# Kernel tuning notes

Measured on AMD Instinct MI355X. Metric: run time of the kernel, lower is better.

The kernel has to match this reference:

```python
import jax, jax.numpy as jnp
import numpy as np

C = 2048
RED = 8
D = C // RED  # 256


def setup_inputs() -> dict:
    key = jax.random.key(0)
    ks = jax.random.split(key, 8)
    n, h, w = 4, 64, 64
    x = jax.random.normal(ks[0], (n, C, h, w), dtype=jnp.float32)
    # 1x1 conv weights stored as [out_ch, in_ch]
    w1 = jax.random.normal(ks[1], (D, C), dtype=jnp.float32) * 0.02
    b1 = jnp.zeros((D,), dtype=jnp.float32)
    w2 = jax.random.normal(ks[2], (D, C), dtype=jnp.float32) * 0.02
    b2 = jnp.zeros((D,), dtype=jnp.float32)
    w3 = jax.random.normal(ks[3], (C, C), dtype=jnp.float32) * 0.02
    b3 = jnp.zeros((C,), dtype=jnp.float32)
    alpha = jnp.zeros((1,), dtype=jnp.float32)
    return {"x": x, "w1": w1, "b1": b1, "w2": w2, "b2": b2,
            "w3": w3, "b3": b3, "alpha": alpha}


def reference(x, w1, b1, w2, b2, w3, b3, alpha):
    n, c, h, w = x.shape
    hw = h * w
    xf = x.reshape(n, c, hw)  # [n, C, HW]
    # 1x1 convs == per-position matmuls over channels
    e1 = jax.nn.relu(jnp.einsum('dc,ncp->ndp', w1, xf) + b1[None, :, None])  # [n, D, HW]
    e2 = jax.nn.relu(jnp.einsum('dc,ncp->ndp', w2, xf) + b2[None, :, None])  # [n, D, HW]
    assembly = jax.nn.relu(jnp.einsum('oc,ncp->nop', w3, xf) + b3[None, :, None])  # [n, C, HW]
    # attention[i, j] = softmax_j( e1[:, i] . e2[:, j] )
    scores = jnp.einsum('ndi,ndj->nij', e1, e2)  # [n, HW, HW]
    attn = jax.nn.softmax(scores, axis=-1)
    # torch.bmm(x, attn^T): out[:, :, i] = sum_j x[:, :, j] * attn[i, j]
    out = jnp.einsum('ncj,nij->nci', xf, attn)  # [n, C, HW]
    y = alpha[0] * out + assembly
    return y.reshape(n, c, h, w)
```

## Files before the change

kernel.cpp:

```cpp
#include <hip/hip_runtime.h>
#include <math.h>

#define CC 2048
#define DD 256
#define PP 4096
#define NB 4

typedef float f32x4 __attribute__((ext_vector_type(4)));
typedef __bf16 bfrag __attribute__((ext_vector_type(8)));

#define AS1(p) ((const __attribute__((address_space(1))) void*)(p))
#define AS3(p) ((__attribute__((address_space(3))) void*)(p))

__device__ __forceinline__ unsigned short f2bf(float f) {
    unsigned int u = __float_as_uint(f);
    u = (u + 0x7fffu + ((u >> 16) & 1u)) >> 16;
    return (unsigned short)u;
}

__global__ __launch_bounds__(256) void prep(const float* __restrict__ x, unsigned short* __restrict__ xT,
                                            const float* __restrict__ w3, unsigned short* __restrict__ w3b) {
    const int t = threadIdx.x;
    if (blockIdx.z == NB) {
        int bid = blockIdx.y * 64 + blockIdx.x;
        int base = (bid * 256 + t) * 8;
#pragma unroll
        for (int j = 0; j < 2; ++j) {
            float4 v = *(const float4*)(w3 + base + j * 4);
            ushort4 r;
            r.x = f2bf(v.x); r.y = f2bf(v.y); r.z = f2bf(v.z); r.w = f2bf(v.w);
            *(ushort4*)(w3b + base + j * 4) = r;
        }
        return;
    }
    __shared__ float tile[64 * 64];
    const int n  = blockIdx.z;
    const int c0 = blockIdx.y * 64;
    const int p0 = blockIdx.x * 64;
    const float* xn = x + (size_t)n * CC * PP;
    {
        const int cl = t >> 4;
        const int g  = t & 15;
        const int pl = g * 4;
#pragma unroll
        for (int ps = 0; ps < 4; ++ps) {
            const int c = cl + ps * 16;
            float4 v = *(const float4*)(xn + (size_t)(c0 + c) * PP + p0 + pl);
            const int gs = g ^ (c >> 2);
            *(float4*)(tile + c * 64 + gs * 4) = v;
        }
    }
    __syncthreads();
    unsigned short* xTn = xT + (size_t)n * PP * CC;
    {
        const int pl2 = t >> 4;
        const int cq  = t & 15;
        const int c4  = cq * 4;
#pragma unroll
        for (int ps = 0; ps < 4; ++ps) {
            const int p  = pl2 + ps * 16;
            const int gs2 = (p >> 2) ^ cq;
            const int base = gs2 * 4 + (p & 3);
            ushort4 r;
            r.x = f2bf(tile[(c4 + 0) * 64 + base]);
            r.y = f2bf(tile[(c4 + 1) * 64 + base]);
            r.z = f2bf(tile[(c4 + 2) * 64 + base]);
            r.w = f2bf(tile[(c4 + 3) * 64 + base]);
            *(ushort4*)(xTn + (size_t)(p0 + p) * CC + c0 + c4) = r;
        }
    }
}

__global__ __launch_bounds__(512, 2) void gemm_assembly(
    const unsigned short* __restrict__ w3b,
    const unsigned short* __restrict__ xT,
    const float* __restrict__ b3,
    float* __restrict__ out)
{
    __shared__ __align__(16) char sm[131072];

    const int t    = threadIdx.x;
    const int wave = t >> 6;
    const int lane = t & 63;
    const int swz  = lane & 7;

    const int p0 = blockIdx.x << 8;
    const int m0 = blockIdx.y << 8;
    const int nb = blockIdx.z;

    const int rA = t >> 3;
    const int g  = (t & 7) ^ (rA & 7);
    const unsigned short* Ag = w3b + (size_t)(m0 + rA) * CC + g * 8;
    const unsigned short* Bg = xT + (size_t)nb * PP * CC + (size_t)(p0 + rA) * CC + g * 8;
    const int ldsw = wave << 10;

    const char* Abase = sm + ((wave >> 2) << 14) + (lane & 15) * 128;
    const char* Bbase = sm + 65536 + (((wave & 3) >> 1) << 14) + ((wave & 1) << 13) + (lane & 15) * 128;

    const int ck0 = (((lane >> 4) ^ swz) << 4);
    const int ck1 = ck0 ^ 0x40;

    f32x4 acc[8][4];
#pragma unroll
    for (int i = 0; i < 8; ++i)
#pragma unroll
        for (int j = 0; j < 4; ++j)
            acc[i][j] = (f32x4){0.f, 0.f, 0.f, 0.f};

    bfrag a0k0, a0k1, a1k0, a1k1, a2k0, a2k1, a3k0, a3k1;
    bfrag bA0k0, bA0k1, bA1k0, bA1k1;
    bfrag bB0k0, bB0k1, bB1k0, bB1k1;

#define STG(SB, DO, kt, h) do { \
    const unsigned short* _s = (SB) + (size_t)(h) * 128 * CC + (size_t)(kt) * 64; \
    char* _d = sm + (DO) + (((kt) & 1) << 15) + ((h) << 14) + ldsw; \
    __builtin_amdgcn_global_load_lds(AS1(_s), AS3(_d), 16, 0, 0); \
    __builtin_amdgcn_global_load_lds(AS1(_s + 64 * CC), AS3(_d + 8192), 16, 0, 0); \
} while (0)

#define LD(dst, BASE, OFF) dst = *(const bfrag*)((BASE) + (OFF))
#define Q(I, J, A_, B_) acc[I][J] = __builtin_amdgcn_mfma_f32_16x16x32_bf16(A_, B_, acc[I][J], 0, 0, 0)
#define BARR __builtin_amdgcn_s_barrier()
#define SB0  __builtin_amdgcn_sched_barrier(0)
#define LG0 do { asm volatile("s_waitcnt lgkmcnt(0)" ::: "memory"); __builtin_amdgcn_sched_barrier(0); } while (0)
#define PRI(x) __builtin_amdgcn_s_setprio(x)

#define TILE(P, kt, IA, IB, VM4, VM0) do { \
    SB0; \
     \
    LD(a0k0, Abase, ((P) << 15) + (0 << 11) + ck0); LD(a0k1, Abase, ((P) << 15) + (0 << 11) + ck1); \
    LD(a1k0, Abase, ((P) << 15) + (1 << 11) + ck0); LD(a1k1, Abase, ((P) << 15) + (1 << 11) + ck1); \
    LD(a2k0, Abase, ((P) << 15) + (2 << 11) + ck0); LD(a2k1, Abase, ((P) << 15) + (2 << 11) + ck1); \
    LD(a3k0, Abase, ((P) << 15) + (3 << 11) + ck0); LD(a3k1, Abase, ((P) << 15) + (3 << 11) + ck1); \
    LD(bA0k0, Bbase, ((P) << 15) + (0 << 11) + ck0); LD(bA0k1, Bbase, ((P) << 15) + (0 << 11) + ck1); \
    LD(bA1k0, Bbase, ((P) << 15) + (1 << 11) + ck0); LD(bA1k1, Bbase, ((P) << 15) + (1 << 11) + ck1); \
    if (IA) STG(Ag, 0, (kt) + 1, 0); \
    SB0; \
    asm volatile("s_waitcnt lgkmcnt(8)" ::: "memory"); \
    BARR; LG0; PRI(1); \
    Q(0, 0, a0k0, bA0k0); Q(1, 0, a1k0, bA0k0); Q(2, 0, a2k0, bA0k0); Q(3, 0, a3k0, bA0k0); \
    Q(0, 1, a0k0, bA1k0); Q(1, 1, a1k0, bA1k0); Q(2, 1, a2k0, bA1k0); Q(3, 1, a3k0, bA1k0); \
    Q(0, 0, a0k1, bA0k1); Q(1, 0, a1k1, bA0k1); Q(2, 0, a2k1, bA0k1); Q(3, 0, a3k1, bA0k1); \
    Q(0, 1, a0k1, bA1k1); Q(1, 1, a1k1, bA1k1); Q(2, 1, a2k1, bA1k1); Q(3, 1, a3k1, bA1k1); \
    PRI(0); BARR; \
     \
    LD(bB0k0, Bbase, ((P) << 15) + (2 << 11) + ck0); LD(bB0k1, Bbase, ((P) << 15) + (2 << 11) + ck1); \
    LD(bB1k0, Bbase, ((P) << 15) + (3 << 11) + ck0); LD(bB1k1, Bbase, ((P) << 15) + (3 << 11) + ck1); \
    if (IA) STG(Ag, 0, (kt) + 1, 1); \
    SB0; \
    BARR; LG0; PRI(1); \
    Q(0, 2, a0k0, bB0k0); Q(1, 2, a1k0, bB0k0); Q(2, 2, a2k0, bB0k0); Q(3, 2, a3k0, bB0k0); \
    Q(0, 3, a0k0, bB1k0); Q(1, 3, a1k0, bB1k0); Q(2, 3, a2k0, bB1k0); Q(3, 3, a3k0, bB1k0); \
    Q(0, 2, a0k1, bB0k1); Q(1, 2, a1k1, bB0k1); Q(2, 2, a2k1, bB0k1); Q(3, 2, a3k1, bB0k1); \
    Q(0, 3, a0k1, bB1k1); Q(1, 3, a1k1, bB1k1); Q(2, 3, a2k1, bB1k1); Q(3, 3, a3k1, bB1k1); \
    PRI(0); BARR; \
     \
    LD(a0k0, Abase, ((P) << 15) + (4 << 11) + ck0); LD(a0k1, Abase, ((P) << 15) + (4 << 11) + ck1); \
    LD(a1k0, Abase, ((P) << 15) + (5 << 11) + ck0); LD(a1k1, Abase, ((P) << 15) + (5 << 11) + ck1); \
    LD(a2k0, Abase, ((P) << 15) + (6 << 11) + ck0); LD(a2k1, Abase, ((P) << 15) + (6 << 11) + ck1); \
    LD(a3k0, Abase, ((P) << 15) + (7 << 11) + ck0); LD(a3k1, Abase, ((P) << 15) + (7 << 11) + ck1); \
    if (IB) STG(Bg, 65536, (kt) + 2, 0); \
    SB0; \
    BARR; LG0; PRI(1); \
    Q(4, 2, a0k0, bB0k0); Q(5, 2, a1k0, bB0k0); Q(6, 2, a2k0, bB0k0); Q(7, 2, a3k0, bB0k0); \
    Q(4, 3, a0k0, bB1k0); Q(5, 3, a1k0, bB1k0); Q(6, 3, a2k0, bB1k0); Q(7, 3, a3k0, bB1k0); \
    Q(4, 2, a0k1, bB0k1); Q(5, 2, a1k1, bB0k1); Q(6, 2, a2k1, bB0k1); Q(7, 2, a3k1, bB0k1); \
    Q(4, 3, a0k1, bB1k1); Q(5, 3, a1k1, bB1k1); Q(6, 3, a2k1, bB1k1); Q(7, 3, a3k1, bB1k1); \
    PRI(0); BARR; \
     \
    if (IB) STG(Bg, 65536, (kt) + 2, 1); \
    SB0; \
    BARR; SB0; PRI(1); \
    Q(4, 0, a0k0, bA0k0); Q(5, 0, a1k0, bA0k0); Q(6, 0, a2k0, bA0k0); Q(7, 0, a3k0, bA0k0); \
    Q(4, 1, a0k0, bA1k0); Q(5, 1, a1k0, bA1k0); Q(6, 1, a2k0, bA1k0); Q(7, 1, a3k0, bA1k0); \
    Q(4, 0, a0k1, bA0k1); Q(5, 0, a1k1, bA0k1); Q(6, 0, a2k1, bA0k1); Q(7, 0, a3k1, bA0k1); \
    Q(4, 1, a0k1, bA1k1); Q(5, 1, a1k1, bA1k1); Q(6, 1, a2k1, bA1k1); Q(7, 1, a3k1, bA1k1); \
    PRI(0); \
    if (VM4) asm volatile("s_waitcnt vmcnt(4)" ::: "memory"); \
    if (VM0) asm volatile("s_waitcnt vmcnt(0)" ::: "memory"); \
    BARR; \
} while (0)

    STG(Ag, 0, 0, 0); STG(Ag, 0, 0, 1);
    STG(Bg, 65536, 0, 0); STG(Bg, 65536, 0, 1);
    STG(Bg, 65536, 1, 0); STG(Bg, 65536, 1, 1);
    asm volatile("s_waitcnt vmcnt(4)" ::: "memory");
    BARR;

#pragma unroll 1
    for (int kt = 0; kt < 30; kt += 2) {
        TILE(0, kt,     1, 1, 1, 0);
        TILE(1, kt + 1, 1, 1, 1, 0);
    }
    TILE(0, 30, 1, 0, 0, 1);
    TILE(1, 31, 0, 0, 0, 0);

#undef TILE
#undef STG
#undef LD
#undef Q
#undef BARR
#undef SB0
#undef LG0
#undef PRI

    const int wr = (wave >> 2) << 7;
    const int wc = (wave & 3) << 6;
    const int q4 = (lane >> 4) << 2;
    const int cl = lane & 15;
    float* outn = out + (size_t)nb * CC * PP;
#pragma unroll
    for (int mi = 0; mi < 8; ++mi) {
#pragma unroll
        for (int r = 0; r < 4; ++r) {
            const int o = m0 + wr + mi * 16 + q4 + r;
            const float bias = b3[o];
            float* orow = outn + (size_t)o * PP + p0 + wc + cl;
#pragma unroll
            for (int ni = 0; ni < 4; ++ni) {
                float v = acc[mi][ni][r] + bias;
                orow[ni * 16] = v > 0.f ? v : 0.f;
            }
        }
    }
}

__global__ void fb_e12(const float* __restrict__ x,
                       const float* __restrict__ w1, const float* __restrict__ b1,
                       const float* __restrict__ w2, const float* __restrict__ b2,
                       const float* __restrict__ alpha,
                       float* __restrict__ e1, float* __restrict__ e2) {
    if (alpha[0] == 0.f) return;
    const size_t total = (size_t)NB * DD * PP;
    for (size_t idx = (size_t)blockIdx.x * blockDim.x + threadIdx.x; idx < total;
         idx += (size_t)gridDim.x * blockDim.x) {
        int p = (int)(idx % PP);
        size_t nd = idx / PP;
        int d = (int)(nd % DD);
        int n = (int)(nd / DD);
        const float* xn = x + (size_t)n * CC * PP + p;
        float s1 = b1[d], s2 = b2[d];
        for (int c = 0; c < CC; ++c) {
            float xv = xn[(size_t)c * PP];
            s1 += w1[(size_t)d * CC + c] * xv;
            s2 += w2[(size_t)d * CC + c] * xv;
        }
        e1[idx] = fmaxf(s1, 0.f);
        e2[idx] = fmaxf(s2, 0.f);
    }
}

__global__ void fb_attn(const float* __restrict__ x,
                        const float* __restrict__ e1, const float* __restrict__ e2,
                        const float* __restrict__ alpha,
                        float* __restrict__ out) {
    const float a = alpha[0];
    if (a == 0.f) return;
    __shared__ float s[PP];
    __shared__ float e1i[DD];
    __shared__ float red[256];
    const int t = threadIdx.x;
    for (int ii = blockIdx.x; ii < NB * PP; ii += gridDim.x) {
        const int n = ii >> 12;
        const int i = ii & (PP - 1);
        const float* e1n = e1 + (size_t)n * DD * PP;
        const float* e2n = e2 + (size_t)n * DD * PP;
        if (t < DD) e1i[t] = e1n[(size_t)t * PP + i];
        __syncthreads();
        for (int j = t; j < PP; j += 256) {
            float acc = 0.f;
            for (int d = 0; d < DD; ++d) acc += e1i[d] * e2n[(size_t)d * PP + j];
            s[j] = acc;
        }
        __syncthreads();
        float m = -INFINITY;
        for (int j = t; j < PP; j += 256) m = fmaxf(m, s[j]);
        red[t] = m; __syncthreads();
        for (int o = 128; o > 0; o >>= 1) { if (t < o) red[t] = fmaxf(red[t], red[t + o]); __syncthreads(); }
        m = red[0]; __syncthreads();
        float l = 0.f;
        for (int j = t; j < PP; j += 256) { float e = __expf(s[j] - m); s[j] = e; l += e; }
        red[t] = l; __syncthreads();
        for (int o = 128; o > 0; o >>= 1) { if (t < o) red[t] += red[t + o]; __syncthreads(); }
        l = red[0]; __syncthreads();
        const float inv = a / l;
        const float* xn = x + (size_t)n * CC * PP;
        float* on = out + (size_t)n * CC * PP;
        for (int c = t; c < CC; c += 256) {
            const float* xr = xn + (size_t)c * PP;
            float acc = 0.f;
            for (int j = 0; j < PP; ++j) acc += s[j] * xr[j];
            on[(size_t)c * PP + i] += inv * acc;
        }
        __syncthreads();
    }
}

extern "C" void kernel_launch(void* const* d_in, const int* in_sizes, int n_in,
                              void* d_out, int out_size, void* d_ws, size_t ws_size,
                              hipStream_t stream) {
    (void)in_sizes; (void)n_in; (void)out_size; (void)ws_size;
    const float* x     = (const float*)d_in[0];
    const float* w1    = (const float*)d_in[1];
    const float* b1    = (const float*)d_in[2];
    const float* w2    = (const float*)d_in[3];
    const float* b2    = (const float*)d_in[4];
    const float* w3    = (const float*)d_in[5];
    const float* b3    = (const float*)d_in[6];
    const float* alpha = (const float*)d_in[7];
    float* out = (float*)d_out;

    unsigned short* xT  = (unsigned short*)d_ws;
    unsigned short* w3b = (unsigned short*)((char*)d_ws + (size_t)NB * PP * CC * 2);
    float* e1 = (float*)d_ws;
    float* e2 = e1 + (size_t)NB * DD * PP;

    prep<<<dim3(PP / 64, CC / 64, NB + 1), dim3(256), 0, stream>>>(x, xT, w3, w3b);
    gemm_assembly<<<dim3(PP / 256, CC / 256, NB), dim3(512), 0, stream>>>(w3b, xT, b3, out);
    fb_e12<<<dim3(512), dim3(256), 0, stream>>>(x, w1, b1, w2, b2, alpha, e1, e2);
    fb_attn<<<dim3(1024), dim3(256), 0, stream>>>(x, e1, e2, alpha, out);
}
```

Baseline: 361.2 us.

## Software-pipeline LDS fragment loads across k-tiles with double-buffered B registers

Restructures the GEMM main loop so the A and B fragments for the next k-tile are read from LDS during the current tile's MFMA phases, with ping-pong B register sets and separate registers for the upper A rows. Waits on LDS counters become partial (lgkmcnt 4/8) instead of full drains, and the vmcnt wait moves earlier inside the tile. The goal is to hide LDS read latency behind MFMAs and cut full-drain stalls, at the cost of more VGPRs and fragile barrier and wait-count ordering.

```diff
diff --git a/kernel.cpp b/kernel.cpp
--- a/kernel.cpp
+++ b/kernel.cpp
@@ -108,8 +108,9 @@
             acc[i][j] = (f32x4){0.f, 0.f, 0.f, 0.f};
 
     bfrag a0k0, a0k1, a1k0, a1k1, a2k0, a2k1, a3k0, a3k1;
-    bfrag bA0k0, bA0k1, bA1k0, bA1k1;
-    bfrag bB0k0, bB0k1, bB1k0, bB1k1;
+    bfrag a4k0, a4k1, a5k0, a5k1, a6k0, a6k1, a7k0, a7k1;
+    bfrag bP0, bP1, bP2, bP3;
+    bfrag bQ0, bQ1, bQ2, bQ3;
 
 #define STG(SB, DO, kt, h) do { \
     const unsigned short* _s = (SB) + (size_t)(h) * 128 * CC + (size_t)(kt) * 64; \
@@ -122,78 +123,88 @@
 #define Q(I, J, A_, B_) acc[I][J] = __builtin_amdgcn_mfma_f32_16x16x32_bf16(A_, B_, acc[I][J], 0, 0, 0)
 #define BARR __builtin_amdgcn_s_barrier()
 #define SB0  __builtin_amdgcn_sched_barrier(0)
-#define LG0 do { asm volatile("s_waitcnt lgkmcnt(0)" ::: "memory"); __builtin_amdgcn_sched_barrier(0); } while (0)
+#define WLG(N) do { asm volatile("s_waitcnt lgkmcnt(" #N ")" ::: "memory"); __builtin_amdgcn_sched_barrier(0); } while (0)
+#define WVM(N) asm volatile("s_waitcnt vmcnt(" #N ")" ::: "memory")
 #define PRI(x) __builtin_amdgcn_s_setprio(x)
 
-#define TILE(P, kt, IA, IB, VM4, VM0) do { \
-    SB0; \
-     \
-    LD(a0k0, Abase, ((P) << 15) + (0 << 11) + ck0); LD(a0k1, Abase, ((P) << 15) + (0 << 11) + ck1); \
-    LD(a1k0, Abase, ((P) << 15) + (1 << 11) + ck0); LD(a1k1, Abase, ((P) << 15) + (1 << 11) + ck1); \
-    LD(a2k0, Abase, ((P) << 15) + (2 << 11) + ck0); LD(a2k1, Abase, ((P) << 15) + (2 << 11) + ck1); \
-    LD(a3k0, Abase, ((P) << 15) + (3 << 11) + ck0); LD(a3k1, Abase, ((P) << 15) + (3 << 11) + ck1); \
-    LD(bA0k0, Bbase, ((P) << 15) + (0 << 11) + ck0); LD(bA0k1, Bbase, ((P) << 15) + (0 << 11) + ck1); \
-    LD(bA1k0, Bbase, ((P) << 15) + (1 << 11) + ck0); LD(bA1k1, Bbase, ((P) << 15) + (1 << 11) + ck1); \
+#define TILE(P, NP, kt, IA, IB, IR, V2, V0, G3, S10,S11,S12,S13, S20,S21,S22,S23) do { \
+     \
+    BARR; SB0; \
+    LD(S20, Bbase, ((P) << 15) + (2 << 11) + ck0); LD(S21, Bbase, ((P) << 15) + (2 << 11) + ck1); \
+    LD(S22, Bbase, ((P) << 15) + (3 << 11) + ck0); LD(S23, Bbase, ((P) << 15) + (3 << 11) + ck1); \
     if (IA) STG(Ag, 0, (kt) + 1, 0); \
-    SB0; \
-    asm volatile("s_waitcnt lgkmcnt(8)" ::: "memory"); \
-    BARR; LG0; PRI(1); \
-    Q(0, 0, a0k0, bA0k0); Q(1, 0, a1k0, bA0k0); Q(2, 0, a2k0, bA0k0); Q(3, 0, a3k0, bA0k0); \
-    Q(0, 1, a0k0, bA1k0); Q(1, 1, a1k0, bA1k0); Q(2, 1, a2k0, bA1k0); Q(3, 1, a3k0, bA1k0); \
-    Q(0, 0, a0k1, bA0k1); Q(1, 0, a1k1, bA0k1); Q(2, 0, a2k1, bA0k1); Q(3, 0, a3k1, bA0k1); \
-    Q(0, 1, a0k1, bA1k1); Q(1, 1, a1k1, bA1k1); Q(2, 1, a2k1, bA1k1); Q(3, 1, a3k1, bA1k1); \
-    PRI(0); BARR; \
-     \
-    LD(bB0k0, Bbase, ((P) << 15) + (2 << 11) + ck0); LD(bB0k1, Bbase, ((P) << 15) + (2 << 11) + ck1); \
-    LD(bB1k0, Bbase, ((P) << 15) + (3 << 11) + ck0); LD(bB1k1, Bbase, ((P) << 15) + (3 << 11) + ck1); \
+    SB0; WLG(4); PRI(1); \
+    Q(0, 0, a0k0, S10); Q(1, 0, a1k0, S10); Q(2, 0, a2k0, S10); Q(3, 0, a3k0, S10); \
+    Q(0, 1, a0k0, S12); Q(1, 1, a1k0, S12); Q(2, 1, a2k0, S12); Q(3, 1, a3k0, S12); \
+    Q(0, 0, a0k1, S11); Q(1, 0, a1k1, S11); Q(2, 0, a2k1, S11); Q(3, 0, a3k1, S11); \
+    Q(0, 1, a0k1, S13); Q(1, 1, a1k1, S13); Q(2, 1, a2k1, S13); Q(3, 1, a3k1, S13); \
+    PRI(0); \
+     \
+    BARR; SB0; \
+    LD(a4k0, Abase, ((P) << 15) + (4 << 11) + ck0); LD(a4k1, Abase, ((P) << 15) + (4 << 11) + ck1); \
+    LD(a5k0, Abase, ((P) << 15) + (5 << 11) + ck0); LD(a5k1, Abase, ((P) << 15) + (5 << 11) + ck1); \
+    LD(a6k0, Abase, ((P) << 15) + (6 << 11) + ck0); LD(a6k1, Abase, ((P) << 15) + (6 << 11) + ck1); \
+    LD(a7k0, Abase, ((P) << 15) + (7 << 11) + ck0); LD(a7k1, Abase, ((P) << 15) + (7 << 11) + ck1); \
     if (IA) STG(Ag, 0, (kt) + 1, 1); \
-    SB0; \
-    BARR; LG0; PRI(1); \
-    Q(0, 2, a0k0, bB0k0); Q(1, 2, a1k0, bB0k0); Q(2, 2, a2k0, bB0k0); Q(3, 2, a3k0, bB0k0); \
-    Q(0, 3, a0k0, bB1k0); Q(1, 3, a1k0, bB1k0); Q(2, 3, a2k0, bB1k0); Q(3, 3, a3k0, bB1k0); \
-    Q(0, 2, a0k1, bB0k1); Q(1, 2, a1k1, bB0k1); Q(2, 2, a2k1, bB0k1); Q(3, 2, a3k1, bB0k1); \
-    Q(0, 3, a0k1, bB1k1); Q(1, 3, a1k1, bB1k1); Q(2, 3, a2k1, bB1k1); Q(3, 3, a3k1, bB1k1); \
-    PRI(0); BARR; \
-     \
-    LD(a0k0, Abase, ((P) << 15) + (4 << 11) + ck0); LD(a0k1, Abase, ((P) << 15) + (4 << 11) + ck1); \
-    LD(a1k0, Abase, ((P) << 15) + (5 << 11) + ck0); LD(a1k1, Abase, ((P) << 15) + (5 << 11) + ck1); \
-    LD(a2k0, Abase, ((P) << 15) + (6 << 11) + ck0); LD(a2k1, Abase, ((P) << 15) + (6 << 11) + ck1); \
-    LD(a3k0, Abase, ((P) << 15) + (7 << 11) + ck0); LD(a3k1, Abase, ((P) << 15) + (7 << 11) + ck1); \
+    SB0; WLG(8); PRI(1); \
+    Q(0, 2, a0k0, S20); Q(1, 2, a1k0, S20); Q(2, 2, a2k0, S20); Q(3, 2, a3k0, S20); \
+    Q(0, 3, a0k0, S22); Q(1, 3, a1k0, S22); Q(2, 3, a2k0, S22); Q(3, 3, a3k0, S22); \
+    Q(0, 2, a0k1, S21); Q(1, 2, a1k1, S21); Q(2, 2, a2k1, S21); Q(3, 2, a3k1, S21); \
+    Q(0, 3, a0k1, S23); Q(1, 3, a1k1, S23); Q(2, 3, a2k1, S23); Q(3, 3, a3k1, S23); \
+    PRI(0); \
+     \
+     \
+    BARR; SB0; \
     if (IB) STG(Bg, 65536, (kt) + 2, 0); \
-    SB0; \
-    BARR; LG0; PRI(1); \
-    Q(4, 2, a0k0, bB0k0); Q(5, 2, a1k0, bB0k0); Q(6, 2, a2k0, bB0k0); Q(7, 2, a3k0, bB0k0); \
-    Q(4, 3, a0k0, bB1k0); Q(5, 3, a1k0, bB1k0); Q(6, 3, a2k0, bB1k0); Q(7, 3, a3k0, bB1k0); \
-    Q(4, 2, a0k1, bB0k1); Q(5, 2, a1k1, bB0k1); Q(6, 2, a2k1, bB0k1); Q(7, 2, a3k1, bB0k1); \
-    Q(4, 3, a0k1, bB1k1); Q(5, 3, a1k1, bB1k1); Q(6, 3, a2k1, bB1k1); Q(7, 3, a3k1, bB1k1); \
-    PRI(0); BARR; \
+    if (V2) WVM(2); \
+    if (V0) WVM(0); \
+    BARR; SB0; \
+    if (IR) { \
+        LD(a0k0, Abase, ((NP) << 15) + (0 << 11) + ck0); LD(a0k1, Abase, ((NP) << 15) + (0 << 11) + ck1); \
+        LD(a1k0, Abase, ((NP) << 15) + (1 << 11) + ck0); LD(a1k1, Abase, ((NP) << 15) + (1 << 11) + ck1); \
+        LD(a2k0, Abase, ((NP) << 15) + (2 << 11) + ck0); LD(a2k1, Abase, ((NP) << 15) + (2 << 11) + ck1); \
+        LD(a3k0, Abase, ((NP) << 15) + (3 << 11) + ck0); LD(a3k1, Abase, ((NP) << 15) + (3 << 11) + ck1); \
+    } \
+    SB0; WLG(G3); PRI(1); \
+    Q(4, 2, a4k0, S20); Q(5, 2, a5k0, S20); Q(6, 2, a6k0, S20); Q(7, 2, a7k0, S20); \
+    Q(4, 3, a4k0, S22); Q(5, 3, a5k0, S22); Q(6, 3, a6k0, S22); Q(7, 3, a7k0, S22); \
+    Q(4, 2, a4k1, S21); Q(5, 2, a5k1, S21); Q(6, 2, a6k1, S21); Q(7, 2, a7k1, S21); \
+    Q(4, 3, a4k1, S23); Q(5, 3, a5k1, S23); Q(6, 3, a6k1, S23); Q(7, 3, a7k1, S23); \
+    PRI(0); \
      \
     if (IB) STG(Bg, 65536, (kt) + 2, 1); \
-    SB0; \
-    BARR; SB0; PRI(1); \
-    Q(4, 0, a0k0, bA0k0); Q(5, 0, a1k0, bA0k0); Q(6, 0, a2k0, bA0k0); Q(7, 0, a3k0, bA0k0); \
-    Q(4, 1, a0k0, bA1k0); Q(5, 1, a1k0, bA1k0); Q(6, 1, a2k0, bA1k0); Q(7, 1, a3k0, bA1k0); \
-    Q(4, 0, a0k1, bA0k1); Q(5, 0, a1k1, bA0k1); Q(6, 0, a2k1, bA0k1); Q(7, 0, a3k1, bA0k1); \
-    Q(4, 1, a0k1, bA1k1); Q(5, 1, a1k1, bA1k1); Q(6, 1, a2k1, bA1k1); Q(7, 1, a3k1, bA1k1); \
+    if (IR) { \
+        LD(S20, Bbase, ((NP) << 15) + (0 << 11) + ck0); LD(S21, Bbase, ((NP) << 15) + (0 << 11) + ck1); \
+        LD(S22, Bbase, ((NP) << 15) + (1 << 11) + ck0); LD(S23, Bbase, ((NP) << 15) + (1 << 11) + ck1); \
+    } \
+    SB0; PRI(1); \
+    Q(4, 0, a4k0, S10); Q(5, 0, a5k0, S10); Q(6, 0, a6k0, S10); Q(7, 0, a7k0, S10); \
+    Q(4, 1, a4k0, S12); Q(5, 1, a5k0, S12); Q(6, 1, a6k0, S12); Q(7, 1, a7k0, S12); \
+    Q(4, 0, a4k1, S11); Q(5, 0, a5k1, S11); Q(6, 0, a6k1, S11); Q(7, 0, a7k1, S11); \
+    Q(4, 1, a4k1, S13); Q(5, 1, a5k1, S13); Q(6, 1, a6k1, S13); Q(7, 1, a7k1, S13); \
     PRI(0); \
-    if (VM4) asm volatile("s_waitcnt vmcnt(4)" ::: "memory"); \
-    if (VM0) asm volatile("s_waitcnt vmcnt(0)" ::: "memory"); \
-    BARR; \
 } while (0)
 
     STG(Ag, 0, 0, 0); STG(Ag, 0, 0, 1);
     STG(Bg, 65536, 0, 0); STG(Bg, 65536, 0, 1);
     STG(Bg, 65536, 1, 0); STG(Bg, 65536, 1, 1);
-    asm volatile("s_waitcnt vmcnt(4)" ::: "memory");
-    BARR;
+    WVM(4);
+    BARR; SB0;
+    LD(a0k0, Abase, (0 << 11) + ck0); LD(a0k1, Abase, (0 << 11) + ck1);
+    LD(a1k0, Abase, (1 << 11) + ck0); LD(a1k1, Abase, (1 << 11) + ck1);
+    LD(a2k0, Abase, (2 << 11) + ck0); LD(a2k1, Abase, (2 << 11) + ck1);
+    LD(a3k0, Abase, (3 << 11) + ck0); LD(a3k1, Abase, (3 << 11) + ck1);
+    LD(bP0, Bbase, (0 << 11) + ck0); LD(bP1, Bbase, (0 << 11) + ck1);
+    LD(bP2, Bbase, (1 << 11) + ck0); LD(bP3, Bbase, (1 << 11) + ck1);
+    SB0;
 
 #pragma unroll 1
     for (int kt = 0; kt < 30; kt += 2) {
-        TILE(0, kt,     1, 1, 1, 0);
-        TILE(1, kt + 1, 1, 1, 1, 0);
-    }
-    TILE(0, 30, 1, 0, 0, 1);
-    TILE(1, 31, 0, 0, 0, 0);
+        TILE(0, 1, kt,     1, 1, 1, 1, 0, 8, bP0, bP1, bP2, bP3, bQ0, bQ1, bQ2, bQ3);
+        TILE(1, 0, kt + 1, 1, 1, 1, 1, 0, 8, bQ0, bQ1, bQ2, bQ3, bP0, bP1, bP2, bP3);
+    }
+    TILE(0, 1, 30, 1, 0, 1, 0, 1, 8, bP0, bP1, bP2, bP3, bQ0, bQ1, bQ2, bQ3);
+    TILE(1, 0, 31, 0, 0, 0, 0, 0, 0, bQ0, bQ1, bQ2, bQ3, bP0, bP1, bP2, bP3);
 
 #undef TILE
 #undef STG
@@ -201,7 +212,8 @@
 #undef Q
 #undef BARR
 #undef SB0
-#undef LG0
+#undef WLG
+#undef WVM
 #undef PRI
 
     const int wr = (wave >> 2) << 7;
```

Measured after the change: 360.0 us. Within noise of the previous version (-0.3%).
